# Performance work log

Measured on AMD Instinct MI355X. Metric: run time of the kernel, lower is better.

Reference implementation:

```python
import jax, jax.numpy as jnp
import numpy as np

BATCH = 1024
H = 1024  # input_size == hidden_size (forced by h0 = z.repeat)
STEPS = 4


def _uniform(key, shape, bound):
    return jax.random.uniform(key, shape, jnp.float32, -bound, bound)


def setup_inputs() -> dict:
    key = jax.random.key(0)
    ks = jax.random.split(key, 12)
    bound = 1.0 / np.sqrt(H)  # PyTorch LSTM/Linear default init range
    return {
        "z": jax.random.normal(ks[0], (BATCH, H), jnp.float32),
        # LSTM layer 0 (gate order: i, f, g, o)
        "W_ih0": _uniform(ks[1], (4 * H, H), bound),
        "W_hh0": _uniform(ks[2], (4 * H, H), bound),
        "b_ih0": _uniform(ks[3], (4 * H,), bound),
        "b_hh0": _uniform(ks[4], (4 * H,), bound),
        # LSTM layer 1
        "W_ih1": _uniform(ks[5], (4 * H, H), bound),
        "W_hh1": _uniform(ks[6], (4 * H, H), bound),
        "b_ih1": _uniform(ks[7], (4 * H,), bound),
        "b_hh1": _uniform(ks[8], (4 * H,), bound),
        # Output linear
        "W_lin": _uniform(ks[9], (H, H), bound),
        "b_lin": _uniform(ks[10], (H,), bound),
    }


def _lstm_cell(x, h, c, W_ih, W_hh, b_ih, b_hh):
    # PyTorch LSTM cell: gates = x W_ih^T + h W_hh^T + b_ih + b_hh, order i,f,g,o
    gates = x @ W_ih.T + h @ W_hh.T + (b_ih + b_hh)
    i, f, g, o = jnp.split(gates, 4, axis=-1)
    c_new = jax.nn.sigmoid(f) * c + jax.nn.sigmoid(i) * jnp.tanh(g)
    h_new = jax.nn.sigmoid(o) * jnp.tanh(c_new)
    return h_new, c_new


def reference(z, W_ih0, W_hh0, b_ih0, b_hh0, W_ih1, W_hh1, b_ih1, b_hh1, W_lin, b_lin):
    # init_hidden: both layers' h and c start as z; input each step is the constant z
    def step(carry, _):
        h0, c0, h1, c1 = carry
        h0, c0 = _lstm_cell(z, h0, c0, W_ih0, W_hh0, b_ih0, b_hh0)
        h1, c1 = _lstm_cell(h0, h1, c1, W_ih1, W_hh1, b_ih1, b_hh1)
        return (h0, c0, h1, c1), h1

    init = (z, z, z, z)
    _, outs = jax.lax.scan(step, init, None, length=STEPS)  # [4, B, H]
    feat = jnp.transpose(outs, (1, 0, 2))  # [B, 4, H]
    return feat @ W_lin.T + b_lin
```

## Files before the change

kernel.cpp:

```cpp
#include <hip/hip_runtime.h>
#include <hip/hip_bf16.h>
#include <cstdint>
#include <cstddef>


typedef __bf16 bf16_t;
typedef __bf16 bf16x8 __attribute__((ext_vector_type(8)));
typedef __bf16 bf16x4 __attribute__((ext_vector_type(4)));
typedef float f32x4 __attribute__((ext_vector_type(4)));

__device__ __forceinline__ void gload_lds16(const bf16_t* g, bf16_t* l) {
    __builtin_amdgcn_global_load_lds(
        (const __attribute__((address_space(1))) void*)g,
        (__attribute__((address_space(3))) void*)l,
        16, 0, 0);
}

__device__ __forceinline__ float sigmoid_f(float x) {
    return 1.f / (1.f + __expf(-x));
}
__device__ __forceinline__ float tanh_fast(float x) {
    const float t = __expf(2.f * x);
    return 1.f - 2.f / (t + 1.f);
}

__device__ __forceinline__ void gemm_core(
    const bf16_t* __restrict__ A, int lda,
    const bf16_t* __restrict__ B, int ldb,
    int K, int brow, int bcol,
    bf16_t* lsA, bf16_t* lsB, f32x4 acc[4][2])
{
    const int tid  = threadIdx.x;
    const int lane = tid & 63;
    const int wave = tid >> 6;
    const int wm = (wave >> 2) * 64;
    const int wn = (wave & 3) * 32;
    const int srow = lane >> 3;
    const int ssw  = ((lane & 7) ^ srow) * 8;
    const int ch0  = wave * 2;
    const int nkt  = K >> 6;

    auto stage = [&](int buf, int ktel) {
#pragma unroll
        for (int it = 0; it < 2; ++it) {
            const int ch = ch0 + it;
            const int row = ch * 8 + srow;
            gload_lds16(A + (size_t)(brow + row) * lda + ktel + ssw, &lsA[buf * 8192 + ch * 512]);
            gload_lds16(B + (size_t)(bcol + row) * ldb + ktel + ssw, &lsB[buf * 8192 + ch * 512]);
        }
    };

    stage(0, 0);
    __syncthreads();

    const int fr  = lane & 15;
    const int g8  = (lane >> 4) * 8;
    const int rsw = (fr & 7) * 8;

    for (int kt = 0; kt < nkt; ++kt) {
        const int buf = kt & 1;
        if (kt + 1 < nkt) stage(buf ^ 1, (kt + 1) << 6);
#pragma unroll
        for (int kk = 0; kk < 2; ++kk) {
            const int ko = (kk * 32 + g8) ^ rsw;
            bf16x8 af[4], bfv[2];
#pragma unroll
            for (int m = 0; m < 4; ++m)
                af[m] = *(const bf16x8*)&lsA[buf * 8192 + (wm + m * 16 + fr) * 64 + ko];
#pragma unroll
            for (int n = 0; n < 2; ++n)
                bfv[n] = *(const bf16x8*)&lsB[buf * 8192 + (wn + n * 16 + fr) * 64 + ko];
#pragma unroll
            for (int m = 0; m < 4; ++m)
#pragma unroll
                for (int n = 0; n < 2; ++n)
                    acc[m][n] = __builtin_amdgcn_mfma_f32_16x16x32_bf16(af[m], bfv[n], acc[m][n], 0, 0, 0);
        }
        __syncthreads();
    }
}

__global__ __launch_bounds__(512) void gemm_bf16_nt(
    const bf16_t* __restrict__ A, int lda, size_t sAz,
    const bf16_t* __restrict__ B, int ldb,
    const float* __restrict__ bias,
    float* __restrict__ C, int ldc, int czoff, int K)
{
    __shared__ __align__(16) bf16_t ls[32768];
    f32x4 acc[4][2] = {};
    const int brow = blockIdx.y * 128;
    const int bcol = blockIdx.x * 128;
    gemm_core(A + (size_t)blockIdx.z * sAz, lda, B, ldb, K, brow, bcol, ls, ls + 16384, acc);

    const int lane = threadIdx.x & 63;
    const int wave = threadIdx.x >> 6;
    const int wm = (wave >> 2) * 64;
    const int wn = (wave & 3) * 32;
    const int cr = (lane >> 4) * 4;
    const int cc = lane & 15;
    const size_t colz = (size_t)blockIdx.z * czoff;
#pragma unroll
    for (int n = 0; n < 2; ++n) {
        const int col = bcol + wn + n * 16 + cc;
        const float bv = bias ? bias[col] : 0.f;
#pragma unroll
        for (int m = 0; m < 4; ++m) {
            const int row0 = brow + wm + m * 16 + cr;
#pragma unroll
            for (int r = 0; r < 4; ++r)
                C[(size_t)(row0 + r) * ldc + colz + col] = acc[m][n][r] + bv;
        }
    }
}

struct FusedArgs {
    const bf16_t* A;
    const bf16_t* B;
    const float*  add;
    const float*  biasR;
    float*        c;
    bf16_t*       h1; int h1s;
    bf16_t*       h2; int h2s;
    int K; int lda;
};

__global__ __launch_bounds__(512, 4) void fused_gemm_cell(FusedArgs fa0, FusedArgs fa1)
{
    __shared__ __align__(16) float gsm[16384];
    const FusedArgs fa = blockIdx.z ? fa1 : fa0;
    const int brow = blockIdx.y * 128;
    const int bcol = blockIdx.x * 128;

    f32x4 acc[4][2] = {};
    bf16_t* ls = (bf16_t*)gsm;
    gemm_core(fa.A, fa.lda, fa.B, fa.K, fa.K, brow, bcol, ls, ls + 16384, acc);

    const int tid  = threadIdx.x;
    const int lane = tid & 63;
    const int wave = tid >> 6;
    const int wm = (wave >> 2) * 64;
    const int wn = (wave & 3) * 32;
    const int cr = (lane >> 4) * 4;
    const int cc = lane & 15;
#pragma unroll
    for (int n = 0; n < 2; ++n)
#pragma unroll
        for (int m = 0; m < 4; ++m)
#pragma unroll
            for (int r = 0; r < 4; ++r)
                gsm[(wm + m * 16 + cr + r) * 128 + wn + n * 16 + cc] = acc[m][n][r];
    __syncthreads();

#pragma unroll
    for (int p = 0; p < 8; ++p) {
        const int idx = p * 512 + tid;
        const int rl = idx >> 5;
        const int nn = idx & 31;
        float4 gv = *(const float4*)&gsm[rl * 128 + nn * 4];
        const int grow = brow + rl;
        const int j0 = bcol + nn * 4;
        if (fa.add) {
            const float4 av = *(const float4*)&fa.add[(size_t)grow * 4096 + j0];
            gv.x += av.x; gv.y += av.y; gv.z += av.z; gv.w += av.w;
        }
        if (fa.biasR) {
            const float4 bv = *(const float4*)&fa.biasR[j0];
            gv.x += bv.x; gv.y += bv.y; gv.z += bv.z; gv.w += bv.w;
        }
        const int ng = j0 >> 2;
        const size_t ci = (size_t)grow * 1024 + ng;
        const float cn = sigmoid_f(gv.y) * fa.c[ci] + sigmoid_f(gv.x) * tanh_fast(gv.z);
        const float h  = sigmoid_f(gv.w) * tanh_fast(cn);
        fa.c[ci] = cn;
        const bf16_t hb = (bf16_t)h;
        fa.h1[(size_t)grow * fa.h1s + ng] = hb;
        if (fa.h2) fa.h2[(size_t)grow * fa.h2s + ng] = hb;
    }
}


__global__ __launch_bounds__(256) void conv_f32_bf16(
    const float4* __restrict__ in, bf16x4* __restrict__ out)
{
    const int t = blockIdx.x * 256 + threadIdx.x;
    const float4 a = in[t];
    bf16x4 v = {(bf16_t)a.x, (bf16_t)a.y, (bf16_t)a.z, (bf16_t)a.w};
    out[t] = v;
}

__global__ __launch_bounds__(256) void convR_f32_bf16(
    const float4* __restrict__ in, bf16x4* __restrict__ out)
{
    const int tid = blockIdx.x * 256 + threadIdx.x;
    const int j = tid >> 8;
    const int col = tid & 255;
    const int g = j & 3, n = j >> 2;
    const float4 a = in[(g * 1024 + n) * 256 + col];
    bf16x4 v = {(bf16_t)a.x, (bf16_t)a.y, (bf16_t)a.z, (bf16_t)a.w};
    out[tid] = v;
}

__global__ __launch_bounds__(256) void prep_wcatR(
    const float4* __restrict__ Wih, const float4* __restrict__ Whh, bf16x4* __restrict__ Wcat)
{
    const int tid = blockIdx.x * 256 + threadIdx.x;
    const int j = tid >> 8;
    const int col = tid & 255;
    const int g = j & 3, n = j >> 2;
    const int src = (g * 1024 + n) * 256 + col;
    const float4 a = Wih[src];
    const float4 b = Whh[src];
    bf16x4 va = {(bf16_t)a.x, (bf16_t)a.y, (bf16_t)a.z, (bf16_t)a.w};
    bf16x4 vb = {(bf16_t)b.x, (bf16_t)b.y, (bf16_t)b.z, (bf16_t)b.w};
    Wcat[j * 512 + col]       = va;
    Wcat[j * 512 + 256 + col] = vb;
}

__global__ __launch_bounds__(256) void prep_biasR(
    const float* __restrict__ bih0, const float* __restrict__ bhh0,
    const float* __restrict__ bih1, const float* __restrict__ bhh1,
    float* __restrict__ b0R, float* __restrict__ b1R)
{
    const int j = blockIdx.x * 256 + threadIdx.x;
    const int g = j & 3, n = j >> 2;
    b0R[j] = bih0[g * 1024 + n] + bhh0[g * 1024 + n];
    b1R[j] = bih1[g * 1024 + n] + bhh1[g * 1024 + n];
}

__global__ __launch_bounds__(256) void prep_init(
    const float* __restrict__ z, bf16_t* __restrict__ zb,
    bf16_t* __restrict__ X0, float* __restrict__ c0, float* __restrict__ c1)
{
    const int tid = blockIdx.x * 256 + threadIdx.x;
    const int b = tid >> 10;
    const int n = tid & 1023;
    const float v = z[tid];
    const bf16_t h = (bf16_t)v;
    zb[tid] = h;
    X0[(size_t)b * 2048 + 1024 + n] = h;
    c0[tid] = v;
    c1[tid] = v;
}

extern "C" void kernel_launch(void* const* d_in, const int* in_sizes, int n_in,
                              void* d_out, int out_size, void* d_ws, size_t ws_size,
                              hipStream_t stream)
{
    const float* z     = (const float*)d_in[0];
    const float* W_ih0 = (const float*)d_in[1];
    const float* W_hh0 = (const float*)d_in[2];
    const float* b_ih0 = (const float*)d_in[3];
    const float* b_hh0 = (const float*)d_in[4];
    const float* W_ih1 = (const float*)d_in[5];
    const float* W_hh1 = (const float*)d_in[6];
    const float* b_ih1 = (const float*)d_in[7];
    const float* b_hh1 = (const float*)d_in[8];
    const float* W_lin = (const float*)d_in[9];
    const float* b_lin = (const float*)d_in[10];
    float* out = (float*)d_out;

    char* ws = (char*)d_ws;
    const size_t MB = 1u << 20;
    bf16_t* WcatR1 = (bf16_t*)(ws);
    bf16_t* Whh0R  = (bf16_t*)(ws + 16 * MB);
    bf16_t* Wih0R  = (bf16_t*)(ws + 24 * MB);
    bf16_t* Wlinb  = (bf16_t*)(ws + 32 * MB);
    bf16_t* zb     = (bf16_t*)(ws + 34 * MB);
    bf16_t* Xbuf   = (bf16_t*)(ws + 36 * MB);
    float*  Gz0R   = (float*) (ws + 44 * MB);
    bf16_t* stash  = (bf16_t*)(ws + 60 * MB);
    float*  c0     = (float*) (ws + 68 * MB);
    float*  c1     = (float*) (ws + 72 * MB);
    float*  bias0R = (float*) (ws + 76 * MB);
    float*  bias1R = (float*) (ws + 76 * MB + 16384);
    bf16_t* X[2] = {Xbuf, Xbuf + (size_t)(1u << 21)};

    convR_f32_bf16<<<4096, 256, 0, stream>>>((const float4*)W_ih0, (bf16x4*)Wih0R);
    convR_f32_bf16<<<4096, 256, 0, stream>>>((const float4*)W_hh0, (bf16x4*)Whh0R);
    prep_wcatR<<<4096, 256, 0, stream>>>((const float4*)W_ih1, (const float4*)W_hh1, (bf16x4*)WcatR1);
    conv_f32_bf16<<<1024, 256, 0, stream>>>((const float4*)W_lin, (bf16x4*)Wlinb);
    prep_biasR<<<16, 256, 0, stream>>>(b_ih0, b_hh0, b_ih1, b_hh1, bias0R, bias1R);
    prep_init<<<4096, 256, 0, stream>>>(z, zb, X[0], c0, c1);

    gemm_bf16_nt<<<dim3(32, 8, 1), 512, 0, stream>>>(zb, 1024, 0, Wih0R, 1024, bias0R, Gz0R, 4096, 0, 1024);

    {
        FusedArgs f0;
        f0.A = zb; f0.lda = 1024; f0.B = Whh0R; f0.add = Gz0R; f0.biasR = nullptr;
        f0.c = c0; f0.h1 = X[0]; f0.h1s = 2048; f0.h2 = nullptr; f0.h2s = 0; f0.K = 1024;
        fused_gemm_cell<<<dim3(32, 8, 1), 512, 0, stream>>>(f0, f0);
    }

    for (int t = 0; t < 4; ++t) {
        const int p = t & 1;
        FusedArgs a0;
        a0.A = X[p]; a0.lda = 2048; a0.B = WcatR1; a0.add = nullptr; a0.biasR = bias1R;
        a0.c = c1; a0.h1 = stash + (size_t)t * (1u << 20); a0.h1s = 1024;
        a0.h2 = (t < 3) ? X[p ^ 1] + 1024 : nullptr; a0.h2s = 2048; a0.K = 2048;
        if (t < 3) {
            FusedArgs a1;
            a1.A = X[p]; a1.lda = 2048; a1.B = Whh0R; a1.add = Gz0R; a1.biasR = nullptr;
            a1.c = c0; a1.h1 = X[p ^ 1]; a1.h1s = 2048; a1.h2 = nullptr; a1.h2s = 0; a1.K = 1024;
            fused_gemm_cell<<<dim3(32, 8, 2), 512, 0, stream>>>(a0, a1);
        } else {
            fused_gemm_cell<<<dim3(32, 8, 1), 512, 0, stream>>>(a0, a0);
        }
    }

    gemm_bf16_nt<<<dim3(8, 8, 4), 512, 0, stream>>>(stash, 1024, (size_t)1 << 20, Wlinb, 1024, b_lin, out, 4096, 1024, 1024);
}
```

Baseline: 224.9 us.

## Merge prep kernels, sum layer-0 weights for step zero, overlap output linear

All weight conversion, bias and init kernels are merged into one prep launch. Because h0 equals z at step zero, that step now uses a precomputed bf16 sum of W_ih0 and W_hh0. That step also runs in the same launch as the Gz GEMM instead of after it. The output linear projection is split per timestep and co-scheduled with the next recurrent step's GEMMs through a generic multi-job kernel with grouped tile ordering, cutting launches and filling idle CUs. The trade-offs are extra weight-sum memory, bf16 rounding of the summed weights, and more runtime branching per block.

Result: faster. 220.1 us (-2.1%).

```diff
diff --git a/kernel.cpp b/kernel.cpp
--- a/kernel.cpp
+++ b/kernel.cpp
@@ -80,60 +80,36 @@
     }
 }
 
-__global__ __launch_bounds__(512) void gemm_bf16_nt(
-    const bf16_t* __restrict__ A, int lda, size_t sAz,
-    const bf16_t* __restrict__ B, int ldb,
-    const float* __restrict__ bias,
-    float* __restrict__ C, int ldc, int czoff, int K)
-{
-    __shared__ __align__(16) bf16_t ls[32768];
-    f32x4 acc[4][2] = {};
-    const int brow = blockIdx.y * 128;
-    const int bcol = blockIdx.x * 128;
-    gemm_core(A + (size_t)blockIdx.z * sAz, lda, B, ldb, K, brow, bcol, ls, ls + 16384, acc);
-
-    const int lane = threadIdx.x & 63;
-    const int wave = threadIdx.x >> 6;
-    const int wm = (wave >> 2) * 64;
-    const int wn = (wave & 3) * 32;
-    const int cr = (lane >> 4) * 4;
-    const int cc = lane & 15;
-    const size_t colz = (size_t)blockIdx.z * czoff;
-#pragma unroll
-    for (int n = 0; n < 2; ++n) {
-        const int col = bcol + wn + n * 16 + cc;
-        const float bv = bias ? bias[col] : 0.f;
-#pragma unroll
-        for (int m = 0; m < 4; ++m) {
-            const int row0 = brow + wm + m * 16 + cr;
-#pragma unroll
-            for (int r = 0; r < 4; ++r)
-                C[(size_t)(row0 + r) * ldc + colz + col] = acc[m][n][r] + bv;
-        }
-    }
-}
-
-struct FusedArgs {
+struct Job {
     const bf16_t* A;
     const bf16_t* B;
     const float*  add;
-    const float*  biasR;
+    const float*  bias;
     float*        c;
-    bf16_t*       h1; int h1s;
-    bf16_t*       h2; int h2s;
-    int K; int lda;
+    bf16_t*       h1;
+    bf16_t*       h2;
+    float*        C;
+    int lda, K, h1s, h2s, mode;
 };
 
-__global__ __launch_bounds__(512, 4) void fused_gemm_cell(FusedArgs fa0, FusedArgs fa1)
+__global__ __launch_bounds__(512, 4) void fused_multi(Job j0, Job j1, Job j2, int n0, int n01)
 {
     __shared__ __align__(16) float gsm[16384];
-    const FusedArgs fa = blockIdx.z ? fa1 : fa0;
-    const int brow = blockIdx.y * 128;
-    const int bcol = blockIdx.x * 128;
+
+    const int bid = blockIdx.x;
+    Job ja; int local, n;
+    if (bid < n0)        { ja = j0; local = bid;       n = n0; }
+    else if (bid < n01)  { ja = j1; local = bid - n0;  n = n01 - n0; }
+    else                 { ja = j2; local = bid - n01; n = (int)gridDim.x - n01; }
+
+    const int q    = n >> 3;
+    const int tile = (local & 7) * q + (local >> 3);
+    const int bcol = (tile >> 3) * 128;
+    const int brow = (tile & 7) * 128;
 
     f32x4 acc[4][2] = {};
     bf16_t* ls = (bf16_t*)gsm;
-    gemm_core(fa.A, fa.lda, fa.B, fa.K, fa.K, brow, bcol, ls, ls + 16384, acc);
+    gemm_core(ja.A, ja.lda, ja.B, ja.K, ja.K, brow, bcol, ls, ls + 16384, acc);
 
     const int tid  = threadIdx.x;
     const int lane = tid & 63;
@@ -142,13 +118,30 @@
     const int wn = (wave & 3) * 32;
     const int cr = (lane >> 4) * 4;
     const int cc = lane & 15;
-#pragma unroll
-    for (int n = 0; n < 2; ++n)
+
+    if (ja.mode == 1) {
+#pragma unroll
+        for (int nn = 0; nn < 2; ++nn) {
+            const int col = bcol + wn + nn * 16 + cc;
+            const float bv = ja.bias ? ja.bias[col] : 0.f;
+#pragma unroll
+            for (int m = 0; m < 4; ++m) {
+                const int row0 = brow + wm + m * 16 + cr;
+#pragma unroll
+                for (int r = 0; r < 4; ++r)
+                    ja.C[(size_t)(row0 + r) * 4096 + col] = acc[m][nn][r] + bv;
+            }
+        }
+        return;
+    }
+
+#pragma unroll
+    for (int nn = 0; nn < 2; ++nn)
 #pragma unroll
         for (int m = 0; m < 4; ++m)
 #pragma unroll
             for (int r = 0; r < 4; ++r)
-                gsm[(wm + m * 16 + cr + r) * 128 + wn + n * 16 + cc] = acc[m][n][r];
+                gsm[(wm + m * 16 + cr + r) * 128 + wn + nn * 16 + cc] = acc[m][nn][r];
     __syncthreads();
 
 #pragma unroll
@@ -158,88 +151,88 @@
         const int nn = idx & 31;
         float4 gv = *(const float4*)&gsm[rl * 128 + nn * 4];
         const int grow = brow + rl;
-        const int j0 = bcol + nn * 4;
-        if (fa.add) {
-            const float4 av = *(const float4*)&fa.add[(size_t)grow * 4096 + j0];
+        const int j0c = bcol + nn * 4;
+        if (ja.add) {
+            const float4 av = *(const float4*)&ja.add[(size_t)grow * 4096 + j0c];
             gv.x += av.x; gv.y += av.y; gv.z += av.z; gv.w += av.w;
         }
-        if (fa.biasR) {
-            const float4 bv = *(const float4*)&fa.biasR[j0];
+        if (ja.bias) {
+            const float4 bv = *(const float4*)&ja.bias[j0c];
             gv.x += bv.x; gv.y += bv.y; gv.z += bv.z; gv.w += bv.w;
         }
-        const int ng = j0 >> 2;
+        const int ng = j0c >> 2;
         const size_t ci = (size_t)grow * 1024 + ng;
-        const float cn = sigmoid_f(gv.y) * fa.c[ci] + sigmoid_f(gv.x) * tanh_fast(gv.z);
+        const float cn = sigmoid_f(gv.y) * ja.c[ci] + sigmoid_f(gv.x) * tanh_fast(gv.z);
         const float h  = sigmoid_f(gv.w) * tanh_fast(cn);
-        fa.c[ci] = cn;
+        ja.c[ci] = cn;
         const bf16_t hb = (bf16_t)h;
-        fa.h1[(size_t)grow * fa.h1s + ng] = hb;
-        if (fa.h2) fa.h2[(size_t)grow * fa.h2s + ng] = hb;
-    }
-}
-
-
-__global__ __launch_bounds__(256) void conv_f32_bf16(
-    const float4* __restrict__ in, bf16x4* __restrict__ out)
+        ja.h1[(size_t)grow * ja.h1s + ng] = hb;
+        if (ja.h2) ja.h2[(size_t)grow * ja.h2s + ng] = hb;
+    }
+}
+
+__global__ __launch_bounds__(256) void prep_all(
+    const float* __restrict__ z,
+    const float4* __restrict__ Wih0, const float4* __restrict__ Whh0,
+    const float4* __restrict__ Wih1, const float4* __restrict__ Whh1,
+    const float4* __restrict__ Wlin,
+    const float* __restrict__ bih0, const float* __restrict__ bhh0,
+    const float* __restrict__ bih1, const float* __restrict__ bhh1,
+    bf16x4* __restrict__ Wih0R, bf16x4* __restrict__ Whh0R, bf16x4* __restrict__ Wsum0R,
+    bf16x4* __restrict__ WcatR1, bf16x4* __restrict__ Wlinb,
+    bf16_t* __restrict__ zb, bf16_t* __restrict__ X0,
+    float* __restrict__ c0, float* __restrict__ c1,
+    float* __restrict__ b0R, float* __restrict__ b1R)
 {
     const int t = blockIdx.x * 256 + threadIdx.x;
-    const float4 a = in[t];
-    bf16x4 v = {(bf16_t)a.x, (bf16_t)a.y, (bf16_t)a.z, (bf16_t)a.w};
-    out[t] = v;
-}
-
-__global__ __launch_bounds__(256) void convR_f32_bf16(
-    const float4* __restrict__ in, bf16x4* __restrict__ out)
-{
-    const int tid = blockIdx.x * 256 + threadIdx.x;
-    const int j = tid >> 8;
-    const int col = tid & 255;
-    const int g = j & 3, n = j >> 2;
-    const float4 a = in[(g * 1024 + n) * 256 + col];
-    bf16x4 v = {(bf16_t)a.x, (bf16_t)a.y, (bf16_t)a.z, (bf16_t)a.w};
-    out[tid] = v;
-}
-
-__global__ __launch_bounds__(256) void prep_wcatR(
-    const float4* __restrict__ Wih, const float4* __restrict__ Whh, bf16x4* __restrict__ Wcat)
-{
-    const int tid = blockIdx.x * 256 + threadIdx.x;
-    const int j = tid >> 8;
-    const int col = tid & 255;
-    const int g = j & 3, n = j >> 2;
-    const int src = (g * 1024 + n) * 256 + col;
-    const float4 a = Wih[src];
-    const float4 b = Whh[src];
-    bf16x4 va = {(bf16_t)a.x, (bf16_t)a.y, (bf16_t)a.z, (bf16_t)a.w};
-    bf16x4 vb = {(bf16_t)b.x, (bf16_t)b.y, (bf16_t)b.z, (bf16_t)b.w};
-    Wcat[j * 512 + col]       = va;
-    Wcat[j * 512 + 256 + col] = vb;
-}
-
-__global__ __launch_bounds__(256) void prep_biasR(
-    const float* __restrict__ bih0, const float* __restrict__ bhh0,
-    const float* __restrict__ bih1, const float* __restrict__ bhh1,
-    float* __restrict__ b0R, float* __restrict__ b1R)
-{
-    const int j = blockIdx.x * 256 + threadIdx.x;
-    const int g = j & 3, n = j >> 2;
-    b0R[j] = bih0[g * 1024 + n] + bhh0[g * 1024 + n];
-    b1R[j] = bih1[g * 1024 + n] + bhh1[g * 1024 + n];
-}
-
-__global__ __launch_bounds__(256) void prep_init(
-    const float* __restrict__ z, bf16_t* __restrict__ zb,
-    bf16_t* __restrict__ X0, float* __restrict__ c0, float* __restrict__ c1)
-{
-    const int tid = blockIdx.x * 256 + threadIdx.x;
-    const int b = tid >> 10;
-    const int n = tid & 1023;
-    const float v = z[tid];
-    const bf16_t h = (bf16_t)v;
-    zb[tid] = h;
-    X0[(size_t)b * 2048 + 1024 + n] = h;
-    c0[tid] = v;
-    c1[tid] = v;
+    if (t < 1048576) {
+        const int j = t >> 8, col = t & 255;
+        const int g = j & 3, nn = j >> 2;
+        const int src = (g * 1024 + nn) * 256 + col;
+        const float4 a = Wih0[src];
+        const float4 b = Whh0[src];
+        bf16x4 va = {(bf16_t)a.x, (bf16_t)a.y, (bf16_t)a.z, (bf16_t)a.w};
+        bf16x4 vb = {(bf16_t)b.x, (bf16_t)b.y, (bf16_t)b.z, (bf16_t)b.w};
+        bf16x4 vs = {(bf16_t)(a.x + b.x), (bf16_t)(a.y + b.y),
+                     (bf16_t)(a.z + b.z), (bf16_t)(a.w + b.w)};
+        Wih0R[t] = va; Whh0R[t] = vb; Wsum0R[t] = vs;
+    } else if (t < 2097152) {
+        const int i = t - 1048576;
+        const int j = i >> 8, col = i & 255;
+        const int g = j & 3, nn = j >> 2;
+        const int src = (g * 1024 + nn) * 256 + col;
+        const float4 a = Wih1[src];
+        const float4 b = Whh1[src];
+        bf16x4 va = {(bf16_t)a.x, (bf16_t)a.y, (bf16_t)a.z, (bf16_t)a.w};
+        bf16x4 vb = {(bf16_t)b.x, (bf16_t)b.y, (bf16_t)b.z, (bf16_t)b.w};
+        WcatR1[j * 512 + col]       = va;
+        WcatR1[j * 512 + 256 + col] = vb;
+    } else if (t < 2359296) {
+        const int i = t - 2097152;
+        const float4 a = Wlin[i];
+        bf16x4 v = {(bf16_t)a.x, (bf16_t)a.y, (bf16_t)a.z, (bf16_t)a.w};
+        Wlinb[i] = v;
+    } else if (t < 2621440) {
+        const int i = t - 2359296;
+        const int b = i >> 8, n4 = i & 255;
+        const float4 v = ((const float4*)z)[i];
+        bf16x4 hv = {(bf16_t)v.x, (bf16_t)v.y, (bf16_t)v.z, (bf16_t)v.w};
+        ((bf16x4*)zb)[i] = hv;
+        *(bf16x4*)(X0 + (size_t)b * 2048 + 1024 + n4 * 4) = hv;
+        ((float4*)c0)[i] = v;
+        ((float4*)c1)[i] = v;
+    } else if (t < 2622464) {
+        const int nn = t - 2621440;
+        float4 b0, b1;
+        float* p0 = (float*)&b0; float* p1 = (float*)&b1;
+#pragma unroll
+        for (int g = 0; g < 4; ++g) {
+            p0[g] = bih0[g * 1024 + nn] + bhh0[g * 1024 + nn];
+            p1[g] = bih1[g * 1024 + nn] + bhh1[g * 1024 + nn];
+        }
+        ((float4*)b0R)[nn] = b0;
+        ((float4*)b1R)[nn] = b1;
+    }
 }
 
 extern "C" void kernel_launch(void* const* d_in, const int* in_sizes, int n_in,
@@ -264,48 +257,70 @@
     bf16_t* WcatR1 = (bf16_t*)(ws);
     bf16_t* Whh0R  = (bf16_t*)(ws + 16 * MB);
     bf16_t* Wih0R  = (bf16_t*)(ws + 24 * MB);
-    bf16_t* Wlinb  = (bf16_t*)(ws + 32 * MB);
-    bf16_t* zb     = (bf16_t*)(ws + 34 * MB);
-    bf16_t* Xbuf   = (bf16_t*)(ws + 36 * MB);
-    float*  Gz0R   = (float*) (ws + 44 * MB);
-    bf16_t* stash  = (bf16_t*)(ws + 60 * MB);
-    float*  c0     = (float*) (ws + 68 * MB);
-    float*  c1     = (float*) (ws + 72 * MB);
-    float*  bias0R = (float*) (ws + 76 * MB);
-    float*  bias1R = (float*) (ws + 76 * MB + 16384);
+    bf16_t* Wsum0R = (bf16_t*)(ws + 32 * MB);
+    bf16_t* Wlinb  = (bf16_t*)(ws + 40 * MB);
+    bf16_t* zb     = (bf16_t*)(ws + 42 * MB);
+    bf16_t* Xbuf   = (bf16_t*)(ws + 44 * MB);
+    float*  Gz0R   = (float*) (ws + 52 * MB);
+    bf16_t* stash  = (bf16_t*)(ws + 68 * MB);
+    float*  c0     = (float*) (ws + 76 * MB);
+    float*  c1     = (float*) (ws + 80 * MB);
+    float*  bias0R = (float*) (ws + 84 * MB);
+    float*  bias1R = (float*) (ws + 84 * MB + 16384);
     bf16_t* X[2] = {Xbuf, Xbuf + (size_t)(1u << 21)};
 
-    convR_f32_bf16<<<4096, 256, 0, stream>>>((const float4*)W_ih0, (bf16x4*)Wih0R);
-    convR_f32_bf16<<<4096, 256, 0, stream>>>((const float4*)W_hh0, (bf16x4*)Whh0R);
-    prep_wcatR<<<4096, 256, 0, stream>>>((const float4*)W_ih1, (const float4*)W_hh1, (bf16x4*)WcatR1);
-    conv_f32_bf16<<<1024, 256, 0, stream>>>((const float4*)W_lin, (bf16x4*)Wlinb);
-    prep_biasR<<<16, 256, 0, stream>>>(b_ih0, b_hh0, b_ih1, b_hh1, bias0R, bias1R);
-    prep_init<<<4096, 256, 0, stream>>>(z, zb, X[0], c0, c1);
-
-    gemm_bf16_nt<<<dim3(32, 8, 1), 512, 0, stream>>>(zb, 1024, 0, Wih0R, 1024, bias0R, Gz0R, 4096, 0, 1024);
+    prep_all<<<10244, 256, 0, stream>>>(
+        z, (const float4*)W_ih0, (const float4*)W_hh0,
+        (const float4*)W_ih1, (const float4*)W_hh1, (const float4*)W_lin,
+        b_ih0, b_hh0, b_ih1, b_hh1,
+        (bf16x4*)Wih0R, (bf16x4*)Whh0R, (bf16x4*)Wsum0R,
+        (bf16x4*)WcatR1, (bf16x4*)Wlinb,
+        zb, X[0], c0, c1, bias0R, bias1R);
+
+    Job empty = {};
 
     {
-        FusedArgs f0;
-        f0.A = zb; f0.lda = 1024; f0.B = Whh0R; f0.add = Gz0R; f0.biasR = nullptr;
-        f0.c = c0; f0.h1 = X[0]; f0.h1s = 2048; f0.h2 = nullptr; f0.h2s = 0; f0.K = 1024;
-        fused_gemm_cell<<<dim3(32, 8, 1), 512, 0, stream>>>(f0, f0);
+        Job gz = {};
+        gz.A = zb; gz.lda = 1024; gz.B = Wih0R; gz.K = 1024;
+        gz.bias = bias0R; gz.C = Gz0R; gz.mode = 1;
+        Job f00 = {};
+        f00.A = zb; f00.lda = 1024; f00.B = Wsum0R; f00.K = 1024;
+        f00.bias = bias0R; f00.c = c0; f00.h1 = X[0]; f00.h1s = 2048; f00.mode = 0;
+        fused_multi<<<512, 512, 0, stream>>>(gz, f00, empty, 256, 512);
     }
 
     for (int t = 0; t < 4; ++t) {
         const int p = t & 1;
-        FusedArgs a0;
-        a0.A = X[p]; a0.lda = 2048; a0.B = WcatR1; a0.add = nullptr; a0.biasR = bias1R;
-        a0.c = c1; a0.h1 = stash + (size_t)t * (1u << 20); a0.h1s = 1024;
-        a0.h2 = (t < 3) ? X[p ^ 1] + 1024 : nullptr; a0.h2s = 2048; a0.K = 2048;
+        Job a0 = {};
+        a0.A = X[p]; a0.lda = 2048; a0.B = WcatR1; a0.K = 2048;
+        a0.bias = bias1R; a0.c = c1;
+        a0.h1 = stash + (size_t)t * (1u << 20); a0.h1s = 1024;
+        if (t < 3) { a0.h2 = X[p ^ 1] + 1024; a0.h2s = 2048; }
+        a0.mode = 0;
+
+        Job a1 = {};
         if (t < 3) {
-            FusedArgs a1;
-            a1.A = X[p]; a1.lda = 2048; a1.B = Whh0R; a1.add = Gz0R; a1.biasR = nullptr;
-            a1.c = c0; a1.h1 = X[p ^ 1]; a1.h1s = 2048; a1.h2 = nullptr; a1.h2s = 0; a1.K = 1024;
-            fused_gemm_cell<<<dim3(32, 8, 2), 512, 0, stream>>>(a0, a1);
-        } else {
-            fused_gemm_cell<<<dim3(32, 8, 1), 512, 0, stream>>>(a0, a0);
-        }
-    }
-
-    gemm_bf16_nt<<<dim3(8, 8, 4), 512, 0, stream>>>(stash, 1024, (size_t)1 << 20, Wlinb, 1024, b_lin, out, 4096, 1024, 1024);
-}
+            a1.A = X[p]; a1.lda = 2048; a1.B = Whh0R; a1.K = 1024;
+            a1.add = Gz0R; a1.c = c0; a1.h1 = X[p ^ 1]; a1.h1s = 2048; a1.mode = 0;
+        }
+
+        Job lj = {};
+        if (t >= 1) {
+            lj.A = stash + (size_t)(t - 1) * (1u << 20); lj.lda = 1024;
+            lj.B = Wlinb; lj.K = 1024; lj.bias = b_lin;
+            lj.C = out + (size_t)(t - 1) * 1024; lj.mode = 1;
+        }
+
+        if (t == 0)      fused_multi<<<512, 512, 0, stream>>>(a0, a1, empty, 256, 512);
+        else if (t < 3)  fused_multi<<<576, 512, 0, stream>>>(a0, a1, lj, 256, 512);
+        else             fused_multi<<<320, 512, 0, stream>>>(a0, lj, empty, 256, 320);
+    }
+
+    {
+        Job lj = {};
+        lj.A = stash + (size_t)3 * (1u << 20); lj.lda = 1024;
+        lj.B = Wlinb; lj.K = 1024; lj.bias = b_lin;
+        lj.C = out + (size_t)3 * 1024; lj.mode = 1;
+        fused_multi<<<64, 512, 0, stream>>>(lj, empty, empty, 64, 64);
+    }
+}
```
